# Kernel tuning notes

Measured on AMD Instinct MI355X. Metric: run time of the kernel, lower is better.

The kernel has to match this reference:

```python
import jax, jax.numpy as jnp
import numpy as np

NB = 5  # frequency bands


def _ln(x, g, b, eps=1e-5):
    m = jnp.mean(x, axis=-1, keepdims=True)
    v = jnp.var(x, axis=-1, keepdims=True)
    return (x - m) / jnp.sqrt(v + eps) * g + b


def _graph_adj(x, adj_w, sw1, sb1, sw2, sb2, pos_factor, pos_enc):
    # x: [B, D, N] -> degree-normalized adjacency [B, N, N]
    d = x.shape[1]
    xt = jnp.swapaxes(x, 1, 2)  # [B, N, D]
    # concat-MLP first layer split: cat(xi, xj) @ W1 == xi @ W1[:d] + xj @ W1[d:]
    a = xt @ sw1[:d]
    bpart = xt @ sw1[d:]
    h = jax.nn.elu(a[:, :, None, :] + bpart[:, None, :, :] + sb1)  # [B, N, N, H]
    dyn = jax.nn.sigmoid(jnp.squeeze(h @ sw2, -1) + sb2)  # [B, N, N]
    static = jax.nn.softmax(adj_w, axis=-1)
    pos = jax.nn.softmax(pos_enc, axis=-1)
    comb = jax.nn.softmax(static + dyn + pos_factor * pos, axis=-1)
    deg = jnp.sum(comb, axis=-1)
    dis = (deg + 1e-8) ** -0.5
    return dis[:, :, None] * comb * dis[:, None, :]


def _gcn(x, adj, w, b):
    # x: [B, D, N], adj: [B, N, N] -> [B, D_out, N]
    xt = jnp.swapaxes(x, 1, 2)
    out = jnp.einsum('bij,bjd->bid', adj, xt) @ w + b
    return jnp.swapaxes(out, 1, 2)


def _mha(x, qkv_w, qkv_b, ow, ob, nh=4):
    B, S, D = x.shape
    dh = D // nh
    q, k, v = jnp.split(x @ qkv_w + qkv_b, 3, axis=-1)
    q = q.reshape(B, S, nh, dh)
    k = k.reshape(B, S, nh, dh)
    v = v.reshape(B, S, nh, dh)
    att = jax.nn.softmax(jnp.einsum('bihd,bjhd->bhij', q, k) / float(np.sqrt(dh)), axis=-1)
    o = jnp.einsum('bhij,bjhd->bihd', att, v).reshape(B, S, D)
    return o @ ow + ob


def setup_inputs():
    key = jax.random.key(0)
    B, D, N = 16, 256, 64
    ks = iter(jax.random.split(key, 40))

    def rn(shape, s=0.05):
        return jax.random.normal(next(ks), shape, dtype=jnp.float32) * s

    eyeN = jnp.eye(N, dtype=jnp.float32)
    return dict(
        feature=jax.random.normal(next(ks), (B, NB * D, 1, N), dtype=jnp.float32),
        l_adj_w=jnp.tile(eyeN[None], (NB, 1, 1)),
        l_sim_w1=rn((NB, 2 * D, D)), l_sim_b1=jnp.zeros((NB, D), jnp.float32),
        l_sim_w2=rn((NB, D, 1)), l_sim_b2=jnp.zeros((NB, 1), jnp.float32),
        l_pos_factor=jnp.full((NB,), 0.5, jnp.float32),
        l_pos_enc=jnp.tile(eyeN[None], (NB, 1, 1)),
        l_gcn_w=rn((NB, D, D)), l_gcn_b=jnp.zeros((NB, D), jnp.float32),
        g_adj_w=jnp.eye(NB, dtype=jnp.float32),
        g_sim_w1=rn((2 * D, D)), g_sim_b1=jnp.zeros((D,), jnp.float32),
        g_sim_w2=rn((D, 1)), g_sim_b2=jnp.zeros((1,), jnp.float32),
        g_pos_factor=jnp.float32(0.5),
        g_pos_enc=jnp.eye(NB, dtype=jnp.float32),
        g_gcn_w=rn((D, D)), g_gcn_b=jnp.zeros((D,), jnp.float32),
        qkv_w=rn((D, 3 * D)), qkv_b=jnp.zeros((3 * D,), jnp.float32),
        attn_ow=rn((D, D)), attn_ob=jnp.zeros((D,), jnp.float32),
        ln1_g=jnp.ones((D,), jnp.float32), ln1_b=jnp.zeros((D,), jnp.float32),
        ln2_g=jnp.ones((D,), jnp.float32), ln2_b=jnp.zeros((D,), jnp.float32),
        mlp_w1=rn((D, 4 * D)), mlp_b1=jnp.zeros((4 * D,), jnp.float32),
        mlp_w2=rn((4 * D, D)), mlp_b2=jnp.zeros((D,), jnp.float32),
        imp_w=rn((NB, N, 1)), imp_b=jnp.zeros((NB, 1), jnp.float32),
    )


def reference(feature, l_adj_w, l_sim_w1, l_sim_b1, l_sim_w2, l_sim_b2,
              l_pos_factor, l_pos_enc, l_gcn_w, l_gcn_b,
              g_adj_w, g_sim_w1, g_sim_b1, g_sim_w2, g_sim_b2,
              g_pos_factor, g_pos_enc, g_gcn_w, g_gcn_b,
              qkv_w, qkv_b, attn_ow, attn_ob,
              ln1_g, ln1_b, ln2_g, ln2_b,
              mlp_w1, mlp_b1, mlp_w2, mlp_b2,
              imp_w, imp_b):
    B = feature.shape[0]
    D = l_gcn_w.shape[-1]
    N = feature.shape[-1]
    # [B, 5*D, 1, N] -> [5, B, D, N] band-major
    x5 = jnp.moveaxis(feature.reshape(B, NB, D, N), 1, 0)
    # per-band local graphs + GCNs (vmapped over the 5 bands)
    local_adj = jax.vmap(_graph_adj)(x5, l_adj_w, l_sim_w1, l_sim_b1,
                                     l_sim_w2, l_sim_b2, l_pos_factor, l_pos_enc)
    local_out = jax.vmap(_gcn)(x5, local_adj, l_gcn_w, l_gcn_b)  # [5, B, D, N]
    scale_nodes = jnp.moveaxis(jnp.mean(local_out, axis=-1), 0, 1)  # [B, 5, D]
    # cross-band attention block (pre: MHA + residual + LN, then MLP + residual + LN)
    attn = _mha(scale_nodes, qkv_w, qkv_b, attn_ow, attn_ob)
    h1 = _ln(scale_nodes + attn, ln1_g, ln1_b)
    mlp = jax.nn.gelu(h1 @ mlp_w1 + mlp_b1, approximate=False) @ mlp_w2 + mlp_b2
    se = _ln(h1 + mlp, ln2_g, ln2_b)  # [B, 5, D]
    # global scale graph over the 5 band nodes
    xg = jnp.swapaxes(se, 1, 2)  # [B, D, 5]
    g_adj = _graph_adj(xg, g_adj_w, g_sim_w1, g_sim_b1, g_sim_w2, g_sim_b2,
                       g_pos_factor, g_pos_enc)
    g_out = jnp.swapaxes(_gcn(xg, g_adj, g_gcn_w, g_gcn_b), 1, 2)  # [B, 5, D]
    # modulate each local band feature by its global scale vector
    enh = local_out * jnp.moveaxis(g_out, 1, 0)[..., None]  # [5, B, D, N]
    # per-band importance projection over channels: [5, B, D, 1]
    out5 = jnp.einsum('kbdn,kno->kbdo', enh, imp_w) + imp_b[:, None, None, :]
    output = jnp.moveaxis(out5, 0, 1).reshape(B, NB * D, 1, 1)
    return output, g_adj, jnp.moveaxis(local_out, 0, 1)
```

## Files before the change

kernel.cpp:

```cpp
#include <hip/hip_runtime.h>
#include <hip/hip_bf16.h>

#define NBANDS 5
#define BATCH  16
#define DIM    256
#define NNODE  64
#define SEQ    5

typedef __hip_bfloat16 bf16;
typedef unsigned short ushort_t;
typedef __attribute__((ext_vector_type(8))) short short8;
typedef __attribute__((ext_vector_type(4))) float float4v;

#define MFMA __builtin_amdgcn_mfma_f32_16x16x32_bf16

__device__ __forceinline__ float bu2f(ushort_t u){
    bf16 h = *reinterpret_cast<bf16*>(&u);
    return __bfloat162float(h);
}
__device__ __forceinline__ ushort_t f2bu(float x){
    bf16 h = __float2bfloat16(x);
    return *reinterpret_cast<ushort_t*>(&h);
}
__device__ __forceinline__ float elu(float v){
    return (v > 0.f) ? v : (__expf(v) - 1.f);
}

__global__ void __launch_bounds__(256) k_head(
    const float* __restrict__ l_adj_w, const float* __restrict__ l_pos_enc,
    const float* __restrict__ l_pf,
    const float* __restrict__ g_adj_w, const float* __restrict__ g_pos_enc,
    const float* __restrict__ g_pf,
    float* __restrict__ sbase, float* __restrict__ gbase,
    const float* __restrict__ w1, const float* __restrict__ gw,
    ushort_t* __restrict__ w1bt, ushort_t* __restrict__ gwbt)
{
    int blk = blockIdx.x;
    int tid = threadIdx.x;
    __shared__ ushort_t tile[64][65];

    if (blk < 80) {
        int r = blk*4 + (tid>>6);
        int k = r >> 6, i = r & 63;
        int t = tid & 63;
        float aw = l_adj_w[(k*NNODE + i)*NNODE + t];
        float pe = l_pos_enc[(k*NNODE + i)*NNODE + t];
        float m1 = aw, m2 = pe;
        for (int o=32;o>0;o>>=1){ m1 = fmaxf(m1, __shfl_xor(m1,o,64)); m2 = fmaxf(m2, __shfl_xor(m2,o,64)); }
        float e1 = __expf(aw-m1), e2 = __expf(pe-m2);
        float s1=e1, s2=e2;
        for (int o=32;o>0;o>>=1){ s1 += __shfl_xor(s1,o,64); s2 += __shfl_xor(s2,o,64); }
        float pf = l_pf[k];
        sbase[(k*NNODE+i)*NNODE + t] = e1/s1 + pf*(e2/s2);
    } else if (blk == 80) {
        if (tid < NBANDS) {
            int i = tid;
            float r1[NBANDS], r2[NBANDS];
            float m1=-1e30f, m2=-1e30f;
            for (int j=0;j<NBANDS;j++){
                r1[j]=g_adj_w[i*NBANDS+j]; r2[j]=g_pos_enc[i*NBANDS+j];
                m1=fmaxf(m1,r1[j]); m2=fmaxf(m2,r2[j]);
            }
            float s1=0.f,s2=0.f;
            for (int j=0;j<NBANDS;j++){ r1[j]=__expf(r1[j]-m1); r2[j]=__expf(r2[j]-m2); s1+=r1[j]; s2+=r2[j]; }
            float pf = g_pf[0];
            for (int j=0;j<NBANDS;j++) gbase[i*NBANDS+j] = r1[j]/s1 + pf*(r2[j]/s2);
        }
    } else {
        int idx = blk - 81;
        int inst = idx >> 4;
        int t = idx & 15;
        int r0 = (t>>2)*64, c0 = (t&3)*64;
        const float* src; ushort_t* dst;
        if (inst < 10){
            int k = inst>>1, half = inst&1;
            src = w1  + ((size_t)k*512 + half*256)*256;
            dst = w1bt+ ((size_t)k*512 + half*256)*256;
        } else {
            int k = inst-10;
            src = gw  + (size_t)k*65536;
            dst = gwbt+ (size_t)k*65536;
        }
        int jj = tid & 63, i4 = tid >> 6;
        for (int p=0;p<16;p++){
            int i = p*4 + i4;
            tile[i][jj] = f2bu(src[(size_t)(r0+i)*256 + c0 + jj]);
        }
        __syncthreads();
        for (int p=0;p<16;p++){
            int i = p*4 + i4;
            dst[(size_t)(c0+i)*256 + r0 + jj] = tile[jj][i];
        }
    }
}

__global__ void __launch_bounds__(512) k_graph(
    const float* __restrict__ feat,
    const ushort_t* __restrict__ w1bt, const float* __restrict__ b1,
    const float* __restrict__ w2, const float* __restrict__ b2arr,
    const float* __restrict__ sbase,
    const ushort_t* __restrict__ gwbt, const float* __restrict__ gb,
    const float* __restrict__ imp_w,
    float* __restrict__ out_local,
    float* __restrict__ scalew4, float* __restrict__ impw4)
{
    int kb = blockIdx.x % 80;
    int iq = blockIdx.x / 80;
    int k  = kb >> 4;
    int b  = kb & 15;
    int i0 = iq << 4;
    int tid = threadIdx.x;
    int w = tid >> 6, lane = tid & 63, c16 = lane & 15, quad = lane >> 4;

    __shared__ ushort_t Ubuf[64*266 + 8];
    __shared__ ushort_t as[16][264];
    __shared__ ushort_t cs[16][72];
    __shared__ ushort_t ys[16][264];
    __shared__ float w2s[DIM];

    const float* src = feat + ((size_t)b*NBANDS + k)*DIM*NNODE;

    int il0 = w*2, il1 = w*2 + 1;
    float sb0 = sbase[(k*NNODE + i0 + il0)*NNODE + lane];
    float sb1 = sbase[(k*NNODE + i0 + il1)*NNODE + lane];
    float sbias2 = b2arr[k];

    if (tid < DIM) w2s[tid] = w2[k*DIM + tid];
    #pragma unroll
    for (int u = 0; u < 32; ++u){
        int idx = u*512 + tid;
        Ubuf[(idx & 63)*264 + (idx >> 6)] = f2bu(src[idx]);
    }
    __syncthreads();

    int col0 = w*32 + c16;
    int col1 = col0 + 16;

    const ushort_t* Ba = w1bt + (size_t)k*512*DIM;
    const ushort_t* Bb = Ba + 256*DIM;
    float4v z = {0.f,0.f,0.f,0.f};
    float4v aA0=z, aA1=z;
    float4v aB00=z,aB01=z,aB10=z,aB11=z,aB20=z,aB21=z,aB30=z,aB31=z;
    #pragma unroll
    for (int ks = 0; ks < 8; ++ks){
        int ko = ks*32 + quad*8;
        short8 fa = *reinterpret_cast<const short8*>(&Ubuf[(i0 + c16)*264 + ko]);
        short8 f0 = *reinterpret_cast<const short8*>(&Ubuf[( 0 + c16)*264 + ko]);
        short8 f1 = *reinterpret_cast<const short8*>(&Ubuf[(16 + c16)*264 + ko]);
        short8 f2 = *reinterpret_cast<const short8*>(&Ubuf[(32 + c16)*264 + ko]);
        short8 f3 = *reinterpret_cast<const short8*>(&Ubuf[(48 + c16)*264 + ko]);
        short8 wa0 = *reinterpret_cast<const short8*>(Ba + (size_t)col0*DIM + ko);
        short8 wa1 = *reinterpret_cast<const short8*>(Ba + (size_t)col1*DIM + ko);
        short8 wb0 = *reinterpret_cast<const short8*>(Bb + (size_t)col0*DIM + ko);
        short8 wb1 = *reinterpret_cast<const short8*>(Bb + (size_t)col1*DIM + ko);
        aA0  = MFMA(fa, wa0, aA0, 0,0,0);
        aA1  = MFMA(fa, wa1, aA1, 0,0,0);
        aB00 = MFMA(f0, wb0, aB00, 0,0,0);
        aB01 = MFMA(f0, wb1, aB01, 0,0,0);
        aB10 = MFMA(f1, wb0, aB10, 0,0,0);
        aB11 = MFMA(f1, wb1, aB11, 0,0,0);
        aB20 = MFMA(f2, wb0, aB20, 0,0,0);
        aB21 = MFMA(f2, wb1, aB21, 0,0,0);
        aB30 = MFMA(f3, wb0, aB30, 0,0,0);
        aB31 = MFMA(f3, wb1, aB31, 0,0,0);
    }
    __syncthreads();
    {
        float bias0 = b1[k*DIM + col0];
        float bias1 = b1[k*DIM + col1];
        int r0 = quad*4;
        #pragma unroll
        for (int r = 0; r < 4; ++r){
            as[r0 + r][col0] = f2bu(aA0[r] + bias0);
            as[r0 + r][col1] = f2bu(aA1[r] + bias1);
            Ubuf[( 0 + r0 + r)*266 + col0] = f2bu(aB00[r]);
            Ubuf[( 0 + r0 + r)*266 + col1] = f2bu(aB01[r]);
            Ubuf[(16 + r0 + r)*266 + col0] = f2bu(aB10[r]);
            Ubuf[(16 + r0 + r)*266 + col1] = f2bu(aB11[r]);
            Ubuf[(32 + r0 + r)*266 + col0] = f2bu(aB20[r]);
            Ubuf[(32 + r0 + r)*266 + col1] = f2bu(aB21[r]);
            Ubuf[(48 + r0 + r)*266 + col0] = f2bu(aB30[r]);
            Ubuf[(48 + r0 + r)*266 + col1] = f2bu(aB31[r]);
        }
    }
    __syncthreads();

    {
        const ushort_t* bd = Ubuf + 266*lane;
        const ushort_t* a0p = as[il0];
        const ushort_t* a1p = as[il1];
        float acc0 = 0.f, acc1 = 0.f;
        #pragma unroll 4
        for (int dd = 0; dd < 64; ++dd){
            unsigned int blo = *reinterpret_cast<const unsigned int*>(bd + dd*4);
            unsigned int bhi = *reinterpret_cast<const unsigned int*>(bd + dd*4 + 2);
            ushort4 a0 = *reinterpret_cast<const ushort4*>(a0p + dd*4);
            ushort4 a1 = *reinterpret_cast<const ushort4*>(a1p + dd*4);
            float4 wv  = *reinterpret_cast<const float4*>(&w2s[dd*4]);
            float bx = bu2f((ushort_t)(blo & 0xffffu));
            float by = bu2f((ushort_t)(blo >> 16));
            float bz = bu2f((ushort_t)(bhi & 0xffffu));
            float bq = bu2f((ushort_t)(bhi >> 16));
            acc0 += elu(bu2f(a0.x)+bx)*wv.x + elu(bu2f(a0.y)+by)*wv.y
                  + elu(bu2f(a0.z)+bz)*wv.z + elu(bu2f(a0.w)+bq)*wv.w;
            acc1 += elu(bu2f(a1.x)+bx)*wv.x + elu(bu2f(a1.y)+by)*wv.y
                  + elu(bu2f(a1.z)+bz)*wv.z + elu(bu2f(a1.w)+bq)*wv.w;
        }
        float sg0 = 1.f/(1.f + __expf(-(acc0 + sbias2)));
        float sg1 = 1.f/(1.f + __expf(-(acc1 + sbias2)));
        float val0 = sb0 + sg0;
        float val1 = sb1 + sg1;
        float m0 = val0, m1 = val1;
        for (int o=32;o>0;o>>=1){ m0 = fmaxf(m0, __shfl_xor(m0,o,64)); m1 = fmaxf(m1, __shfl_xor(m1,o,64)); }
        float e0 = __expf(val0 - m0), e1 = __expf(val1 - m1);
        float s0 = e0, s1 = e1;
        for (int o=32;o>0;o>>=1){ s0 += __shfl_xor(s0,o,64); s1 += __shfl_xor(s1,o,64); }
        cs[il0][lane] = f2bu(e0/s0);
        cs[il1][lane] = f2bu(e1/s1);
    }
    __syncthreads();

    float4v aY0 = z, aY1 = z;
    {
        #pragma unroll
        for (int ks = 0; ks < 2; ++ks){
            int ko = ks*32 + quad*8;
            short8 af = *reinterpret_cast<const short8*>(&cs[c16][ko]);
            const float* f0p = src + (size_t)col0*NNODE + ko;
            const float* f1p = src + (size_t)col1*NNODE + ko;
            float4 x0 = *reinterpret_cast<const float4*>(f0p);
            float4 x1 = *reinterpret_cast<const float4*>(f0p+4);
            float4 y0 = *reinterpret_cast<const float4*>(f1p);
            float4 y1 = *reinterpret_cast<const float4*>(f1p+4);
            short8 bf0, bf1;
            bf0[0]=(short)f2bu(x0.x); bf0[1]=(short)f2bu(x0.y); bf0[2]=(short)f2bu(x0.z); bf0[3]=(short)f2bu(x0.w);
            bf0[4]=(short)f2bu(x1.x); bf0[5]=(short)f2bu(x1.y); bf0[6]=(short)f2bu(x1.z); bf0[7]=(short)f2bu(x1.w);
            bf1[0]=(short)f2bu(y0.x); bf1[1]=(short)f2bu(y0.y); bf1[2]=(short)f2bu(y0.z); bf1[3]=(short)f2bu(y0.w);
            bf1[4]=(short)f2bu(y1.x); bf1[5]=(short)f2bu(y1.y); bf1[6]=(short)f2bu(y1.z); bf1[7]=(short)f2bu(y1.w);
            aY0 = MFMA(af, bf0, aY0, 0,0,0);
            aY1 = MFMA(af, bf1, aY1, 0,0,0);
        }
        #pragma unroll
        for (int r=0;r<4;++r){
            ys[quad*4 + r][col0] = f2bu(aY0[r]);
            ys[quad*4 + r][col1] = f2bu(aY1[r]);
        }
    }
    __syncthreads();

    {
        float4v aG0 = z, aG1 = z;
        const ushort_t* Bg = gwbt + (size_t)k*DIM*DIM;
        #pragma unroll
        for (int ks = 0; ks < 8; ++ks){
            int ko = ks*32 + quad*8;
            short8 af = *reinterpret_cast<const short8*>(&ys[c16][ko]);
            short8 g0 = *reinterpret_cast<const short8*>(Bg + (size_t)col0*DIM + ko);
            short8 g1 = *reinterpret_cast<const short8*>(Bg + (size_t)col1*DIM + ko);
            aG0 = MFMA(af, g0, aG0, 0,0,0);
            aG1 = MFMA(af, g1, aG1, 0,0,0);
        }
        int nb = i0 + quad*4;
        float iw0 = imp_w[k*NNODE + nb + 0];
        float iw1 = imp_w[k*NNODE + nb + 1];
        float iw2 = imp_w[k*NNODE + nb + 2];
        float iw3 = imp_w[k*NNODE + nb + 3];
        size_t obase = ((size_t)b*NBANDS + k)*DIM;

        float bias0 = gb[k*DIM + col0];
        float v0 = aG0[0]+bias0, v1 = aG0[1]+bias0, v2 = aG0[2]+bias0, v3 = aG0[3]+bias0;
        float4 vv = make_float4(v0,v1,v2,v3);
        *reinterpret_cast<float4*>(&out_local[(obase + col0)*NNODE + nb]) = vv;
        float s  = v0+v1+v2+v3;
        float di = v0*iw0 + v1*iw1 + v2*iw2 + v3*iw3;
        s  += __shfl_xor(s,16,64);  s  += __shfl_xor(s,32,64);
        di += __shfl_xor(di,16,64); di += __shfl_xor(di,32,64);
        if (quad == 0){
            size_t o = ((size_t)iq*80 + b*SEQ + k)*DIM + col0;
            scalew4[o] = s;
            impw4[o]   = di;
        }

        float bias1 = gb[k*DIM + col1];
        v0 = aG1[0]+bias1; v1 = aG1[1]+bias1; v2 = aG1[2]+bias1; v3 = aG1[3]+bias1;
        vv = make_float4(v0,v1,v2,v3);
        *reinterpret_cast<float4*>(&out_local[(obase + col1)*NNODE + nb]) = vv;
        s  = v0+v1+v2+v3;
        di = v0*iw0 + v1*iw1 + v2*iw2 + v3*iw3;
        s  += __shfl_xor(s,16,64);  s  += __shfl_xor(s,32,64);
        di += __shfl_xor(di,16,64); di += __shfl_xor(di,32,64);
        if (quad == 0){
            size_t o = ((size_t)iq*80 + b*SEQ + k)*DIM + col1;
            scalew4[o] = s;
            impw4[o]   = di;
        }
    }
}

__global__ void __launch_bounds__(256) k_qkv_gemv(const float* __restrict__ scalew4,
                        const float* __restrict__ w, const float* __restrict__ bias,
                        float* __restrict__ out)
{
    int row = blockIdx.x / 12;
    int n0 = (blockIdx.x % 12) * 64;
    int tid = threadIdx.x;
    int c = tid & 63, s = tid >> 6;
    __shared__ float xs[DIM];
    __shared__ float part[4][64];
    {
        size_t basei = (size_t)row*DIM + tid;
        xs[tid] = (scalew4[basei] + scalew4[20480 + basei]
                 + scalew4[40960 + basei] + scalew4[61440 + basei]) * (1.f/64.f);
    }
    __syncthreads();
    const float* wp = w + (size_t)(s*64)*768 + n0 + c;
    const float* xp = xs + s*64;
    float acc = 0.f;
    #pragma unroll 8
    for (int i = 0; i < 64; ++i) acc += xp[i] * wp[(size_t)i*768];
    part[s][c] = acc;
    __syncthreads();
    if (s == 0){
        out[(size_t)row*768 + n0 + c] = bias[n0+c] + part[0][c]+part[1][c]+part[2][c]+part[3][c];
    }
}

template<int COLS, int SLICES>
__global__ void __launch_bounds__(256) k_gemv(const float* __restrict__ x, const float* __restrict__ w,
                       const float* __restrict__ bias, float* __restrict__ out,
                       int K, int N, int act)
{
    int chunks = N / COLS;
    int row = blockIdx.x / chunks;
    int n0 = (blockIdx.x % chunks) * COLS;
    int c = threadIdx.x % COLS, s = threadIdx.x / COLS;
    __shared__ float xs[1024];
    __shared__ float part[SLICES][COLS];
    for (int i = threadIdx.x; i < K; i += 256) xs[i] = x[(size_t)row*K + i];
    __syncthreads();
    int klen = K / SLICES;
    const float* wp = w + (size_t)(s*klen)*N + n0 + c;
    const float* xp = xs + s*klen;
    float acc = 0.f;
    #pragma unroll 8
    for (int i = 0; i < klen; ++i) acc += xp[i] * wp[(size_t)i*N];
    part[s][c] = acc;
    __syncthreads();
    if (s == 0){
        float v = bias[n0+c];
        #pragma unroll
        for (int q=0;q<SLICES;q++) v += part[q][c];
        if (act) v = 0.5f*v*(1.f + erff(v*0.70710678118654752f));
        out[(size_t)row*N + n0 + c] = v;
    }
}

__global__ void __launch_bounds__(256) k_projattn(const float* __restrict__ qkvw,
                        const float* __restrict__ ow, const float* __restrict__ ob,
                        float* __restrict__ projw)
{
    int row = blockIdx.x / 4;
    int n0 = (blockIdx.x % 4) * 64;
    int b = row / SEQ, i = row % SEQ;
    int tid = threadIdx.x;
    int h = tid >> 6, l = tid & 63;
    __shared__ float xs[DIM];
    __shared__ float part[4][64];
    const float* base = qkvw + (size_t)b*SEQ*3*DIM;
    float qv = base[(size_t)i*3*DIM + h*64 + l];
    float pj[SEQ];
    #pragma unroll
    for (int j=0;j<SEQ;j++){
        float p = qv * base[(size_t)j*3*DIM + DIM + h*64 + l];
        for (int o=32;o>0;o>>=1) p += __shfl_xor(p,o,64);
        pj[j] = p * 0.125f;
    }
    float m = pj[0];
    #pragma unroll
    for (int j=1;j<SEQ;j++) m = fmaxf(m, pj[j]);
    float ssum = 0.f;
    #pragma unroll
    for (int j=0;j<SEQ;j++){ pj[j] = __expf(pj[j]-m); ssum += pj[j]; }
    float inv = 1.f/ssum;
    float o = 0.f;
    #pragma unroll
    for (int j=0;j<SEQ;j++) o += pj[j]*inv * base[(size_t)j*3*DIM + 2*DIM + h*64 + l];
    xs[tid] = o;
    __syncthreads();
    int c = tid & 63, s = tid >> 6;
    const float* wp = ow + (size_t)(s*64)*DIM + n0 + c;
    const float* xp = xs + s*64;
    float acc = 0.f;
    #pragma unroll 8
    for (int k=0;k<64;++k) acc += xp[k] * wp[(size_t)k*DIM];
    part[s][c] = acc;
    __syncthreads();
    if (s == 0){
        projw[(size_t)row*DIM + n0 + c] = ob[n0+c] + part[0][c]+part[1][c]+part[2][c]+part[3][c];
    }
}

__device__ __forceinline__ float block_ln(float v, int tid, float* red, float g, float bln)
{
    float s = v;
    for (int o=32;o>0;o>>=1) s += __shfl_xor(s,o,64);
    int wave = tid>>6, lane = tid&63;
    if (lane==0) red[wave] = s;
    __syncthreads();
    float mean = (red[0]+red[1]+red[2]+red[3]) * (1.f/DIM);
    float c = v - mean;
    float q = c*c;
    for (int o=32;o>0;o>>=1) q += __shfl_xor(q,o,64);
    __syncthreads();
    if (lane==0) red[wave] = q;
    __syncthreads();
    float var = (red[0]+red[1]+red[2]+red[3]) * (1.f/DIM);
    return c * rsqrtf(var + 1e-5f) * g + bln;
}

__global__ void __launch_bounds__(256) k_mlp1_ln(const float* __restrict__ projw,
                         const float* __restrict__ scalew4,
                         const float* __restrict__ ln1_g, const float* __restrict__ ln1_b,
                         const float* __restrict__ w1, const float* __restrict__ b1,
                         float* __restrict__ h1w, float* __restrict__ mhw)
{
    int row = blockIdx.x / 16;
    int n0 = (blockIdx.x % 16) * 64;
    int tid = threadIdx.x;
    __shared__ float xs[DIM];
    __shared__ float red[4];
    __shared__ float part[4][64];
    size_t basei = (size_t)row*DIM + tid;
    float sc = (scalew4[basei] + scalew4[20480 + basei]
              + scalew4[40960 + basei] + scalew4[61440 + basei]) * (1.f/64.f);
    float v = projw[basei] + sc;
    float h = block_ln(v, tid, red, ln1_g[tid], ln1_b[tid]);
    xs[tid] = h;
    if ((blockIdx.x % 16) == 0) h1w[basei] = h;
    __syncthreads();
    int c = tid & 63, s = tid >> 6;
    const float* wp = w1 + (size_t)(s*64)*1024 + n0 + c;
    const float* xp = xs + s*64;
    float acc = 0.f;
    #pragma unroll 8
    for (int i=0;i<64;++i) acc += xp[i] * wp[(size_t)i*1024];
    part[s][c] = acc;
    __syncthreads();
    if (s == 0){
        float o = b1[n0+c] + part[0][c] + part[1][c] + part[2][c] + part[3][c];
        o = 0.5f*o*(1.f + erff(o*0.70710678118654752f));
        mhw[(size_t)row*1024 + n0 + c] = o;
    }
}

__global__ void __launch_bounds__(256) k_gab_ln(const float* __restrict__ m2w,
                        const float* __restrict__ h1w,
                        const float* __restrict__ ln2_g, const float* __restrict__ ln2_b,
                        const float* __restrict__ gw1, const float* __restrict__ gb1,
                        float* __restrict__ sew, float* __restrict__ gaw, float* __restrict__ gbw)
{
    int row = blockIdx.x / 4;
    int n0 = (blockIdx.x % 4) * 64;
    int tid = threadIdx.x;
    __shared__ float xs[DIM];
    __shared__ float red[4];
    __shared__ float partA[4][64];
    __shared__ float partB[4][64];
    float v = m2w[(size_t)row*DIM + tid] + h1w[(size_t)row*DIM + tid];
    float h = block_ln(v, tid, red, ln2_g[tid], ln2_b[tid]);
    xs[tid] = h;
    if ((blockIdx.x % 4) == 0) sew[(size_t)row*DIM + tid] = h;
    __syncthreads();
    int c = tid & 63, s = tid >> 6;
    const float* wpA = gw1 + (size_t)(s*64)*DIM + n0 + c;
    const float* wpB = wpA + (size_t)DIM*DIM;
    const float* xp = xs + s*64;
    float aA = 0.f, aB = 0.f;
    #pragma unroll 8
    for (int i=0;i<64;++i){
        float xv = xp[i];
        aA += xv * wpA[(size_t)i*DIM];
        aB += xv * wpB[(size_t)i*DIM];
    }
    partA[s][c] = aA;
    partB[s][c] = aB;
    __syncthreads();
    if (s == 0){
        gaw[(size_t)row*DIM + n0 + c] = gb1[n0+c] + partA[0][c]+partA[1][c]+partA[2][c]+partA[3][c];
        gbw[(size_t)row*DIM + n0 + c] = partB[0][c]+partB[1][c]+partB[2][c]+partB[3][c];
    }
}

__global__ void __launch_bounds__(256) k_goutfin(const float* __restrict__ gaw,
                        const float* __restrict__ gbw,
                        const float* __restrict__ gw2, const float* __restrict__ gb2,
                        const float* __restrict__ gbase,
                        const float* __restrict__ sew,
                        const float* __restrict__ ggw, const float* __restrict__ ggb,
                        const float* __restrict__ impw4, const float* __restrict__ imp_b,
                        float* __restrict__ out0, float* __restrict__ out_gadj)
{
    int row = blockIdx.x / 4;
    int n0 = (blockIdx.x % 4) * 64;
    int b = row / SEQ, i = row % SEQ;
    int tid = threadIdx.x;
    int wave = tid >> 6, lane = tid & 63;
    __shared__ float dyn_s[SEQ];
    __shared__ float xs[DIM];
    __shared__ float part[4][64];
    for (int j = wave; j < SEQ; j += 4){
        const float* gar = gaw + (size_t)row*DIM;
        const float* gbr = gbw + ((size_t)b*SEQ + j)*DIM;
        float acc = 0.f;
        #pragma unroll
        for (int m=0;m<4;m++){
            int dd = lane + m*64;
            float v = gar[dd] + gbr[dd];
            acc += elu(v) * gw2[dd];
        }
        for (int o=32;o>0;o>>=1) acc += __shfl_xor(acc,o,64);
        if (lane==0) dyn_s[j] = acc;
    }
    __syncthreads();
    float gc[SEQ];
    {
        float sb2 = gb2[0];
        float m = -1e30f;
        #pragma unroll
        for (int j=0;j<SEQ;j++){
            float sg = 1.f/(1.f+__expf(-(dyn_s[j]+sb2)));
            gc[j] = gbase[i*SEQ+j] + sg;
            m = fmaxf(m, gc[j]);
        }
        float ssum=0.f;
        #pragma unroll
        for (int j=0;j<SEQ;j++){ gc[j]=__expf(gc[j]-m); ssum+=gc[j]; }
        float inv = 1.f/ssum;
        #pragma unroll
        for (int j=0;j<SEQ;j++) gc[j] *= inv;
    }
    if (n0 == 0 && tid < SEQ) out_gadj[((size_t)b*SEQ+i)*SEQ + tid] = gc[tid];
    float t = 0.f;
    #pragma unroll
    for (int j=0;j<SEQ;j++) t += gc[j]*sew[((size_t)b*SEQ + j)*DIM + tid];
    xs[tid] = t;
    __syncthreads();
    int c = tid & 63, s = tid >> 6;
    const float* wp = ggw + (size_t)(s*64)*DIM + n0 + c;
    const float* xp = xs + s*64;
    float acc = 0.f;
    #pragma unroll 8
    for (int k=0;k<64;++k) acc += xp[k] * wp[(size_t)k*DIM];
    part[s][c] = acc;
    __syncthreads();
    if (s == 0){
        float g = ggb[n0+c] + part[0][c]+part[1][c]+part[2][c]+part[3][c];
        size_t o = (size_t)row*DIM + n0 + c;
        float imps = impw4[o] + impw4[20480 + o] + impw4[40960 + o] + impw4[61440 + o];
        out0[o] = g * imps + imp_b[i];
    }
}

extern "C" void kernel_launch(void* const* d_in, const int* in_sizes, int n_in,
                              void* d_out, int out_size, void* d_ws, size_t ws_size,
                              hipStream_t stream)
{
    const float* feature      = (const float*)d_in[0];
    const float* l_adj_w      = (const float*)d_in[1];
    const float* l_sim_w1     = (const float*)d_in[2];
    const float* l_sim_b1     = (const float*)d_in[3];
    const float* l_sim_w2     = (const float*)d_in[4];
    const float* l_sim_b2     = (const float*)d_in[5];
    const float* l_pos_factor = (const float*)d_in[6];
    const float* l_pos_enc    = (const float*)d_in[7];
    const float* l_gcn_w      = (const float*)d_in[8];
    const float* l_gcn_b      = (const float*)d_in[9];
    const float* g_adj_w      = (const float*)d_in[10];
    const float* g_sim_w1     = (const float*)d_in[11];
    const float* g_sim_b1     = (const float*)d_in[12];
    const float* g_sim_w2     = (const float*)d_in[13];
    const float* g_sim_b2     = (const float*)d_in[14];
    const float* g_pos_factor = (const float*)d_in[15];
    const float* g_pos_enc    = (const float*)d_in[16];
    const float* g_gcn_w      = (const float*)d_in[17];
    const float* g_gcn_b      = (const float*)d_in[18];
    const float* qkv_w        = (const float*)d_in[19];
    const float* qkv_b        = (const float*)d_in[20];
    const float* attn_ow      = (const float*)d_in[21];
    const float* attn_ob      = (const float*)d_in[22];
    const float* ln1_g        = (const float*)d_in[23];
    const float* ln1_b        = (const float*)d_in[24];
    const float* ln2_g        = (const float*)d_in[25];
    const float* ln2_b        = (const float*)d_in[26];
    const float* mlp_w1       = (const float*)d_in[27];
    const float* mlp_b1       = (const float*)d_in[28];
    const float* mlp_w2       = (const float*)d_in[29];
    const float* mlp_b2       = (const float*)d_in[30];
    const float* imp_w        = (const float*)d_in[31];
    const float* imp_b        = (const float*)d_in[32];

    float* out0      = (float*)d_out;
    float* out_gadj  = out0 + (size_t)BATCH*NBANDS*DIM;
    float* out_local = out_gadj + (size_t)BATCH*NBANDS*NBANDS;

    ushort_t* w1bt = (ushort_t*)d_ws;
    ushort_t* gwbt = w1bt + (size_t)NBANDS*512*DIM;
    float* fp = (float*)(gwbt + (size_t)NBANDS*DIM*DIM);
    float* sbase   = fp; fp += NBANDS*NNODE*NNODE;
    float* gbase   = fp; fp += 32;
    float* scalew4 = fp; fp += 4*BATCH*SEQ*DIM;
    float* impw4   = fp; fp += 4*BATCH*SEQ*DIM;
    float* qkvw    = fp; fp += BATCH*SEQ*3*DIM;
    float* projw   = fp; fp += BATCH*SEQ*DIM;
    float* h1w     = fp; fp += BATCH*SEQ*DIM;
    float* mhw     = fp; fp += BATCH*SEQ*4*DIM;
    float* m2w     = fp; fp += BATCH*SEQ*DIM;
    float* sew     = fp; fp += BATCH*SEQ*DIM;
    float* gaw     = fp; fp += BATCH*SEQ*DIM;
    float* gbw     = fp; fp += BATCH*SEQ*DIM;

    const int ROWS = BATCH*SEQ;

    k_head<<<321, 256, 0, stream>>>(l_adj_w, l_pos_enc, l_pos_factor,
                                    g_adj_w, g_pos_enc, g_pos_factor,
                                    sbase, gbase,
                                    l_sim_w1, l_gcn_w, w1bt, gwbt);
    k_graph<<<NBANDS*BATCH*4, 512, 0, stream>>>(feature, w1bt, l_sim_b1,
                                    l_sim_w2, l_sim_b2, sbase,
                                    gwbt, l_gcn_b, imp_w,
                                    out_local, scalew4, impw4);
    k_qkv_gemv<<<ROWS*12, 256, 0, stream>>>(scalew4, qkv_w, qkv_b, qkvw);
    k_projattn<<<ROWS*4, 256, 0, stream>>>(qkvw, attn_ow, attn_ob, projw);
    k_mlp1_ln<<<ROWS*16, 256, 0, stream>>>(projw, scalew4, ln1_g, ln1_b, mlp_w1, mlp_b1, h1w, mhw);
    k_gemv<32,8><<<ROWS*8, 256, 0, stream>>>(mhw, mlp_w2, mlp_b2, m2w, 1024, 256, 0);
    k_gab_ln<<<ROWS*4, 256, 0, stream>>>(m2w, h1w, ln2_g, ln2_b, g_sim_w1, g_sim_b1, sew, gaw, gbw);
    k_goutfin<<<ROWS*4, 256, 0, stream>>>(gaw, gbw, g_sim_w2, g_sim_b2, gbase,
                                          sew, g_gcn_w, g_gcn_b, impw4, imp_b,
                                          out0, out_gadj);
}
```

Measured before the change: 215.8 us.

## Fuse attention, MLP and layer-norm chain into one per-row kernel

Five small GEMV kernels (QKV, attention+proj, MLP1+LN, MLP2, LN2+graph projection) are merged into one kernel with one 512-thread block per sequence row, and their intermediates stay in shared memory. In k_graph, ys now reuses Ubuf, w2 is read straight from global memory, and the feature transpose load packs 8 bf16 values per store. This removes four launches and their global round trips. The cost is only 80 blocks doing full-width GEMVs with K-loops up to 256 long, so parallelism drops sharply and weight reads are repeated per row.

```diff
diff --git a/kernel.cpp b/kernel.cpp
--- a/kernel.cpp
+++ b/kernel.cpp
@@ -24,6 +24,9 @@
 }
 __device__ __forceinline__ float elu(float v){
     return (v > 0.f) ? v : (__expf(v) - 1.f);
+}
+__device__ __forceinline__ float sum4(const float* __restrict__ p, size_t i){
+    return p[i] + p[20480 + i] + p[40960 + i] + p[61440 + i];
 }
 
 __global__ void __launch_bounds__(256) k_head(
@@ -112,11 +115,10 @@
     int tid = threadIdx.x;
     int w = tid >> 6, lane = tid & 63, c16 = lane & 15, quad = lane >> 4;
 
-    __shared__ ushort_t Ubuf[64*266 + 8];
-    __shared__ ushort_t as[16][264];
-    __shared__ ushort_t cs[16][72];
-    __shared__ ushort_t ys[16][264];
-    __shared__ float w2s[DIM];
+    __shared__ __align__(16) ushort_t Ubuf[64*266 + 8];
+    __shared__ __align__(16) ushort_t as[16][260];
+    __shared__ __align__(16) ushort_t cs[16][72];
+    ushort_t* ys = Ubuf;
 
     const float* src = feat + ((size_t)b*NBANDS + k)*DIM*NNODE;
 
@@ -125,11 +127,15 @@
     float sb1 = sbase[(k*NNODE + i0 + il1)*NNODE + lane];
     float sbias2 = b2arr[k];
 
-    if (tid < DIM) w2s[tid] = w2[k*DIM + tid];
     #pragma unroll
-    for (int u = 0; u < 32; ++u){
-        int idx = u*512 + tid;
-        Ubuf[(idx & 63)*264 + (idx >> 6)] = f2bu(src[idx]);
+    for (int u = 0; u < 4; ++u){
+        int t = u*512 + tid;
+        int n = t & 63;
+        int d0 = (t >> 6) * 8;
+        short8 pk;
+        #pragma unroll
+        for (int i = 0; i < 8; ++i) pk[i] = (short)f2bu(src[(size_t)(d0+i)*NNODE + n]);
+        *reinterpret_cast<short8*>(&Ubuf[(size_t)n*264 + d0]) = pk;
     }
     __syncthreads();
 
@@ -187,8 +193,9 @@
 
     {
         const ushort_t* bd = Ubuf + 266*lane;
-        const ushort_t* a0p = as[il0];
-        const ushort_t* a1p = as[il1];
+        const ushort_t* a0p = &as[il0][0];
+        const ushort_t* a1p = &as[il1][0];
+        const float* w2p = w2 + k*DIM;
         float acc0 = 0.f, acc1 = 0.f;
         #pragma unroll 4
         for (int dd = 0; dd < 64; ++dd){
@@ -196,7 +203,7 @@
             unsigned int bhi = *reinterpret_cast<const unsigned int*>(bd + dd*4 + 2);
             ushort4 a0 = *reinterpret_cast<const ushort4*>(a0p + dd*4);
             ushort4 a1 = *reinterpret_cast<const ushort4*>(a1p + dd*4);
-            float4 wv  = *reinterpret_cast<const float4*>(&w2s[dd*4]);
+            float4 wv  = *reinterpret_cast<const float4*>(w2p + dd*4);
             float bx = bu2f((ushort_t)(blo & 0xffffu));
             float by = bu2f((ushort_t)(blo >> 16));
             float bz = bu2f((ushort_t)(bhi & 0xffffu));
@@ -220,8 +227,8 @@
     }
     __syncthreads();
 
-    float4v aY0 = z, aY1 = z;
-    {
+    {
+        float4v aY0 = z, aY1 = z;
         #pragma unroll
         for (int ks = 0; ks < 2; ++ks){
             int ko = ks*32 + quad*8;
@@ -242,8 +249,8 @@
         }
         #pragma unroll
         for (int r=0;r<4;++r){
-            ys[quad*4 + r][col0] = f2bu(aY0[r]);
-            ys[quad*4 + r][col1] = f2bu(aY1[r]);
+            ys[(quad*4 + r)*264 + col0] = f2bu(aY0[r]);
+            ys[(quad*4 + r)*264 + col1] = f2bu(aY1[r]);
         }
     }
     __syncthreads();
@@ -254,7 +261,7 @@
         #pragma unroll
         for (int ks = 0; ks < 8; ++ks){
             int ko = ks*32 + quad*8;
-            short8 af = *reinterpret_cast<const short8*>(&ys[c16][ko]);
+            short8 af = *reinterpret_cast<const short8*>(&ys[c16*264 + ko]);
             short8 g0 = *reinterpret_cast<const short8*>(Bg + (size_t)col0*DIM + ko);
             short8 g1 = *reinterpret_cast<const short8*>(Bg + (size_t)col1*DIM + ko);
             aG0 = MFMA(af, g0, aG0, 0,0,0);
@@ -269,225 +276,181 @@
 
         float bias0 = gb[k*DIM + col0];
         float v0 = aG0[0]+bias0, v1 = aG0[1]+bias0, v2 = aG0[2]+bias0, v3 = aG0[3]+bias0;
-        float4 vv = make_float4(v0,v1,v2,v3);
-        *reinterpret_cast<float4*>(&out_local[(obase + col0)*NNODE + nb]) = vv;
+        *reinterpret_cast<float4*>(&out_local[(obase + col0)*NNODE + nb]) =
+            make_float4(v0,v1,v2,v3);
         float s  = v0+v1+v2+v3;
         float di = v0*iw0 + v1*iw1 + v2*iw2 + v3*iw3;
         s  += __shfl_xor(s,16,64);  s  += __shfl_xor(s,32,64);
         di += __shfl_xor(di,16,64); di += __shfl_xor(di,32,64);
         if (quad == 0){
-            size_t o = ((size_t)iq*80 + b*SEQ + k)*DIM + col0;
+            size_t o = (size_t)iq*20480 + ((size_t)b*SEQ + k)*DIM + col0;
             scalew4[o] = s;
             impw4[o]   = di;
         }
 
         float bias1 = gb[k*DIM + col1];
         v0 = aG1[0]+bias1; v1 = aG1[1]+bias1; v2 = aG1[2]+bias1; v3 = aG1[3]+bias1;
-        vv = make_float4(v0,v1,v2,v3);
-        *reinterpret_cast<float4*>(&out_local[(obase + col1)*NNODE + nb]) = vv;
+        *reinterpret_cast<float4*>(&out_local[(obase + col1)*NNODE + nb]) =
+            make_float4(v0,v1,v2,v3);
         s  = v0+v1+v2+v3;
         di = v0*iw0 + v1*iw1 + v2*iw2 + v3*iw3;
         s  += __shfl_xor(s,16,64);  s  += __shfl_xor(s,32,64);
         di += __shfl_xor(di,16,64); di += __shfl_xor(di,32,64);
         if (quad == 0){
-            size_t o = ((size_t)iq*80 + b*SEQ + k)*DIM + col1;
+            size_t o = (size_t)iq*20480 + ((size_t)b*SEQ + k)*DIM + col1;
             scalew4[o] = s;
             impw4[o]   = di;
         }
     }
 }
 
-__global__ void __launch_bounds__(256) k_qkv_gemv(const float* __restrict__ scalew4,
-                        const float* __restrict__ w, const float* __restrict__ bias,
-                        float* __restrict__ out)
-{
-    int row = blockIdx.x / 12;
-    int n0 = (blockIdx.x % 12) * 64;
-    int tid = threadIdx.x;
-    int c = tid & 63, s = tid >> 6;
-    __shared__ float xs[DIM];
-    __shared__ float part[4][64];
-    {
-        size_t basei = (size_t)row*DIM + tid;
-        xs[tid] = (scalew4[basei] + scalew4[20480 + basei]
-                 + scalew4[40960 + basei] + scalew4[61440 + basei]) * (1.f/64.f);
-    }
-    __syncthreads();
-    const float* wp = w + (size_t)(s*64)*768 + n0 + c;
-    const float* xp = xs + s*64;
-    float acc = 0.f;
-    #pragma unroll 8
-    for (int i = 0; i < 64; ++i) acc += xp[i] * wp[(size_t)i*768];
-    part[s][c] = acc;
-    __syncthreads();
-    if (s == 0){
-        out[(size_t)row*768 + n0 + c] = bias[n0+c] + part[0][c]+part[1][c]+part[2][c]+part[3][c];
-    }
-}
-
-template<int COLS, int SLICES>
-__global__ void __launch_bounds__(256) k_gemv(const float* __restrict__ x, const float* __restrict__ w,
-                       const float* __restrict__ bias, float* __restrict__ out,
-                       int K, int N, int act)
-{
-    int chunks = N / COLS;
-    int row = blockIdx.x / chunks;
-    int n0 = (blockIdx.x % chunks) * COLS;
-    int c = threadIdx.x % COLS, s = threadIdx.x / COLS;
-    __shared__ float xs[1024];
-    __shared__ float part[SLICES][COLS];
-    for (int i = threadIdx.x; i < K; i += 256) xs[i] = x[(size_t)row*K + i];
-    __syncthreads();
-    int klen = K / SLICES;
-    const float* wp = w + (size_t)(s*klen)*N + n0 + c;
-    const float* xp = xs + s*klen;
-    float acc = 0.f;
-    #pragma unroll 8
-    for (int i = 0; i < klen; ++i) acc += xp[i] * wp[(size_t)i*N];
-    part[s][c] = acc;
-    __syncthreads();
-    if (s == 0){
-        float v = bias[n0+c];
-        #pragma unroll
-        for (int q=0;q<SLICES;q++) v += part[q][c];
-        if (act) v = 0.5f*v*(1.f + erff(v*0.70710678118654752f));
-        out[(size_t)row*N + n0 + c] = v;
-    }
-}
-
-__global__ void __launch_bounds__(256) k_projattn(const float* __restrict__ qkvw,
-                        const float* __restrict__ ow, const float* __restrict__ ob,
-                        float* __restrict__ projw)
-{
-    int row = blockIdx.x / 4;
-    int n0 = (blockIdx.x % 4) * 64;
-    int b = row / SEQ, i = row % SEQ;
-    int tid = threadIdx.x;
-    int h = tid >> 6, l = tid & 63;
-    __shared__ float xs[DIM];
-    __shared__ float part[4][64];
-    const float* base = qkvw + (size_t)b*SEQ*3*DIM;
-    float qv = base[(size_t)i*3*DIM + h*64 + l];
-    float pj[SEQ];
-    #pragma unroll
-    for (int j=0;j<SEQ;j++){
-        float p = qv * base[(size_t)j*3*DIM + DIM + h*64 + l];
-        for (int o=32;o>0;o>>=1) p += __shfl_xor(p,o,64);
-        pj[j] = p * 0.125f;
-    }
-    float m = pj[0];
-    #pragma unroll
-    for (int j=1;j<SEQ;j++) m = fmaxf(m, pj[j]);
-    float ssum = 0.f;
-    #pragma unroll
-    for (int j=0;j<SEQ;j++){ pj[j] = __expf(pj[j]-m); ssum += pj[j]; }
-    float inv = 1.f/ssum;
-    float o = 0.f;
-    #pragma unroll
-    for (int j=0;j<SEQ;j++) o += pj[j]*inv * base[(size_t)j*3*DIM + 2*DIM + h*64 + l];
-    xs[tid] = o;
-    __syncthreads();
-    int c = tid & 63, s = tid >> 6;
-    const float* wp = ow + (size_t)(s*64)*DIM + n0 + c;
-    const float* xp = xs + s*64;
-    float acc = 0.f;
-    #pragma unroll 8
-    for (int k=0;k<64;++k) acc += xp[k] * wp[(size_t)k*DIM];
-    part[s][c] = acc;
-    __syncthreads();
-    if (s == 0){
-        projw[(size_t)row*DIM + n0 + c] = ob[n0+c] + part[0][c]+part[1][c]+part[2][c]+part[3][c];
-    }
-}
-
-__device__ __forceinline__ float block_ln(float v, int tid, float* red, float g, float bln)
+__device__ __forceinline__ float block_ln512(float v, int tid, float* red, float g, float bb)
 {
     float s = v;
     for (int o=32;o>0;o>>=1) s += __shfl_xor(s,o,64);
     int wave = tid>>6, lane = tid&63;
     if (lane==0) red[wave] = s;
     __syncthreads();
-    float mean = (red[0]+red[1]+red[2]+red[3]) * (1.f/DIM);
+    float mean = (red[0]+red[1]+red[2]+red[3]+red[4]+red[5]+red[6]+red[7]) * (1.f/512.f);
     float c = v - mean;
     float q = c*c;
     for (int o=32;o>0;o>>=1) q += __shfl_xor(q,o,64);
     __syncthreads();
     if (lane==0) red[wave] = q;
     __syncthreads();
-    float var = (red[0]+red[1]+red[2]+red[3]) * (1.f/DIM);
-    return c * rsqrtf(var + 1e-5f) * g + bln;
-}
-
-__global__ void __launch_bounds__(256) k_mlp1_ln(const float* __restrict__ projw,
-                         const float* __restrict__ scalew4,
-                         const float* __restrict__ ln1_g, const float* __restrict__ ln1_b,
-                         const float* __restrict__ w1, const float* __restrict__ b1,
-                         float* __restrict__ h1w, float* __restrict__ mhw)
+    float var = (red[0]+red[1]+red[2]+red[3]+red[4]+red[5]+red[6]+red[7]) * (1.f/512.f);
+    return c * rsqrtf(var + 1e-5f) * g + bb;
+}
+
+__global__ void __launch_bounds__(512) k_attnmlp(
+    const float* __restrict__ scalew4,
+    const float* __restrict__ qkv_w, const float* __restrict__ qkv_b,
+    const float* __restrict__ attn_ow, const float* __restrict__ attn_ob,
+    const float* __restrict__ ln1_g, const float* __restrict__ ln1_b,
+    const float* __restrict__ mlp_w1, const float* __restrict__ mlp_b1,
+    const float* __restrict__ mlp_w2, const float* __restrict__ mlp_b2,
+    const float* __restrict__ ln2_g, const float* __restrict__ ln2_b,
+    const float* __restrict__ gw1, const float* __restrict__ gb1,
+    float* __restrict__ sew, float* __restrict__ gaw, float* __restrict__ gbw)
 {
-    int row = blockIdx.x / 16;
-    int n0 = (blockIdx.x % 16) * 64;
+    int r = blockIdx.x;
+    int b = r / SEQ, i = r % SEQ;
     int tid = threadIdx.x;
-    __shared__ float xs[DIM];
-    __shared__ float red[4];
-    __shared__ float part[4][64];
-    size_t basei = (size_t)row*DIM + tid;
-    float sc = (scalew4[basei] + scalew4[20480 + basei]
-              + scalew4[40960 + basei] + scalew4[61440 + basei]) * (1.f/64.f);
-    float v = projw[basei] + sc;
-    float h = block_ln(v, tid, red, ln1_g[tid], ln1_b[tid]);
-    xs[tid] = h;
-    if ((blockIdx.x % 16) == 0) h1w[basei] = h;
-    __syncthreads();
-    int c = tid & 63, s = tid >> 6;
-    const float* wp = w1 + (size_t)(s*64)*1024 + n0 + c;
-    const float* xp = xs + s*64;
-    float acc = 0.f;
-    #pragma unroll 8
-    for (int i=0;i<64;++i) acc += xp[i] * wp[(size_t)i*1024];
-    part[s][c] = acc;
-    __syncthreads();
-    if (s == 0){
-        float o = b1[n0+c] + part[0][c] + part[1][c] + part[2][c] + part[3][c];
-        o = 0.5f*o*(1.f + erff(o*0.70710678118654752f));
-        mhw[(size_t)row*1024 + n0 + c] = o;
-    }
-}
-
-__global__ void __launch_bounds__(256) k_gab_ln(const float* __restrict__ m2w,
-                        const float* __restrict__ h1w,
-                        const float* __restrict__ ln2_g, const float* __restrict__ ln2_b,
-                        const float* __restrict__ gw1, const float* __restrict__ gb1,
-                        float* __restrict__ sew, float* __restrict__ gaw, float* __restrict__ gbw)
-{
-    int row = blockIdx.x / 4;
-    int n0 = (blockIdx.x % 4) * 64;
-    int tid = threadIdx.x;
-    __shared__ float xs[DIM];
-    __shared__ float red[4];
-    __shared__ float partA[4][64];
-    __shared__ float partB[4][64];
-    float v = m2w[(size_t)row*DIM + tid] + h1w[(size_t)row*DIM + tid];
-    float h = block_ln(v, tid, red, ln2_g[tid], ln2_b[tid]);
-    xs[tid] = h;
-    if ((blockIdx.x % 4) == 0) sew[(size_t)row*DIM + tid] = h;
-    __syncthreads();
-    int c = tid & 63, s = tid >> 6;
-    const float* wpA = gw1 + (size_t)(s*64)*DIM + n0 + c;
-    const float* wpB = wpA + (size_t)DIM*DIM;
-    const float* xp = xs + s*64;
-    float aA = 0.f, aB = 0.f;
-    #pragma unroll 8
-    for (int i=0;i<64;++i){
-        float xv = xp[i];
-        aA += xv * wpA[(size_t)i*DIM];
-        aB += xv * wpB[(size_t)i*DIM];
-    }
-    partA[s][c] = aA;
-    partB[s][c] = aB;
-    __syncthreads();
-    if (s == 0){
-        gaw[(size_t)row*DIM + n0 + c] = gb1[n0+c] + partA[0][c]+partA[1][c]+partA[2][c]+partA[3][c];
-        gbw[(size_t)row*DIM + n0 + c] = partB[0][c]+partB[1][c]+partB[2][c]+partB[3][c];
+    int wave = tid >> 6, lane = tid & 63;
+
+    __shared__ float xs5[SEQ][260];
+    __shared__ float kv[2*SEQ][260];
+    __shared__ float qi[260];
+    __shared__ float xo[260];
+    __shared__ float h1s[260];
+    __shared__ float mh[1032];
+    __shared__ float ses[260];
+    __shared__ float parts[2][260];
+    __shared__ float red[8];
+
+    for (int t = tid; t < SEQ*DIM; t += 512){
+        int j = t >> 8, d = t & 255;
+        xs5[j][d] = sum4(scalew4, ((size_t)b*SEQ + j)*DIM + d) * (1.f/64.f);
+    }
+    __syncthreads();
+
+    for (int o = tid; o < 2816; o += 512){
+        int row, colIdx; float* dst;
+        if (o < 256){ row = i; colIdx = o; dst = &qi[o]; }
+        else {
+            int o2 = o - 256;
+            int j = o2 >> 9, c = o2 & 511;
+            row = j; colIdx = 256 + c;
+            dst = (c < 256) ? &kv[j][c] : &kv[SEQ + j][c - 256];
+        }
+        float acc = qkv_b[colIdx];
+        const float* wp = qkv_w + colIdx;
+        const float* xp = xs5[row];
+        #pragma unroll 8
+        for (int d = 0; d < DIM; ++d) acc += xp[d] * wp[(size_t)d*768];
+        *dst = acc;
+    }
+    __syncthreads();
+
+    if (wave < 4){
+        int h = wave;
+        float qv = qi[h*64 + lane];
+        float pj[SEQ];
+        #pragma unroll
+        for (int j=0;j<SEQ;j++){
+            float p = qv * kv[j][h*64 + lane];
+            for (int o=32;o>0;o>>=1) p += __shfl_xor(p,o,64);
+            pj[j] = p * 0.125f;
+        }
+        float m = pj[0];
+        #pragma unroll
+        for (int j=1;j<SEQ;j++) m = fmaxf(m, pj[j]);
+        float ss = 0.f;
+        #pragma unroll
+        for (int j=0;j<SEQ;j++){ pj[j] = __expf(pj[j]-m); ss += pj[j]; }
+        float inv = 1.f/ss;
+        float o = 0.f;
+        #pragma unroll
+        for (int j=0;j<SEQ;j++) o += pj[j]*inv * kv[SEQ + j][h*64 + lane];
+        xo[h*64 + lane] = o;
+    }
+    __syncthreads();
+
+    {
+        int c = tid & 255, s = tid >> 8;
+        const float* wp = attn_ow + (size_t)(s*128)*DIM + c;
+        const float* xp = xo + s*128;
+        float acc = 0.f;
+        #pragma unroll 8
+        for (int kk=0;kk<128;++kk) acc += xp[kk] * wp[(size_t)kk*DIM];
+        parts[s][c] = acc;
+    }
+    __syncthreads();
+    if (tid < 256) h1s[tid] = attn_ob[tid] + parts[0][tid] + parts[1][tid] + xs5[i][tid];
+    __syncthreads();
+    {
+        int c = tid & 255;
+        float h = block_ln512(h1s[c], tid, red, ln1_g[c], ln1_b[c]);
+        if (tid < 256) h1s[c] = h;
+    }
+    __syncthreads();
+
+    for (int o = tid; o < 1024; o += 512){
+        float acc = mlp_b1[o];
+        const float* wp = mlp_w1 + o;
+        #pragma unroll 8
+        for (int d = 0; d < DIM; ++d) acc += h1s[d] * wp[(size_t)d*1024];
+        mh[o] = 0.5f*acc*(1.f + erff(acc*0.70710678118654752f));
+    }
+    __syncthreads();
+
+    {
+        int c = tid & 255, s = tid >> 8;
+        const float* wp = mlp_w2 + (size_t)(s*512)*DIM + c;
+        const float* xp = mh + s*512;
+        float acc = 0.f;
+        #pragma unroll 8
+        for (int kk=0;kk<512;++kk) acc += xp[kk] * wp[(size_t)kk*DIM];
+        parts[s][c] = acc;
+    }
+    __syncthreads();
+    if (tid < 256) ses[tid] = mlp_b2[tid] + parts[0][tid] + parts[1][tid] + h1s[tid];
+    __syncthreads();
+    {
+        int c = tid & 255;
+        float h = block_ln512(ses[c], tid, red, ln2_g[c], ln2_b[c]);
+        if (tid < 256){ ses[c] = h; sew[(size_t)r*DIM + c] = h; }
+    }
+    __syncthreads();
+
+    {
+        int mat = tid >> 8, c = tid & 255;
+        float acc = (mat == 0) ? gb1[c] : 0.f;
+        const float* wp = gw1 + (size_t)(mat*DIM)*DIM + c;
+        #pragma unroll 8
+        for (int d = 0; d < DIM; ++d) acc += ses[d] * wp[(size_t)d*DIM];
+        if (mat == 0) gaw[(size_t)r*DIM + c] = acc;
+        else          gbw[(size_t)r*DIM + c] = acc;
     }
 }
 
@@ -556,7 +519,7 @@
     if (s == 0){
         float g = ggb[n0+c] + part[0][c]+part[1][c]+part[2][c]+part[3][c];
         size_t o = (size_t)row*DIM + n0 + c;
-        float imps = impw4[o] + impw4[20480 + o] + impw4[40960 + o] + impw4[61440 + o];
+        float imps = sum4(impw4, o);
         out0[o] = g * imps + imp_b[i];
     }
 }
@@ -610,11 +573,6 @@
     float* gbase   = fp; fp += 32;
     float* scalew4 = fp; fp += 4*BATCH*SEQ*DIM;
     float* impw4   = fp; fp += 4*BATCH*SEQ*DIM;
-    float* qkvw    = fp; fp += BATCH*SEQ*3*DIM;
-    float* projw   = fp; fp += BATCH*SEQ*DIM;
-    float* h1w     = fp; fp += BATCH*SEQ*DIM;
-    float* mhw     = fp; fp += BATCH*SEQ*4*DIM;
-    float* m2w     = fp; fp += BATCH*SEQ*DIM;
     float* sew     = fp; fp += BATCH*SEQ*DIM;
     float* gaw     = fp; fp += BATCH*SEQ*DIM;
     float* gbw     = fp; fp += BATCH*SEQ*DIM;
@@ -629,11 +587,11 @@
                                     l_sim_w2, l_sim_b2, sbase,
                                     gwbt, l_gcn_b, imp_w,
                                     out_local, scalew4, impw4);
-    k_qkv_gemv<<<ROWS*12, 256, 0, stream>>>(scalew4, qkv_w, qkv_b, qkvw);
-    k_projattn<<<ROWS*4, 256, 0, stream>>>(qkvw, attn_ow, attn_ob, projw);
-    k_mlp1_ln<<<ROWS*16, 256, 0, stream>>>(projw, scalew4, ln1_g, ln1_b, mlp_w1, mlp_b1, h1w, mhw);
-    k_gemv<32,8><<<ROWS*8, 256, 0, stream>>>(mhw, mlp_w2, mlp_b2, m2w, 1024, 256, 0);
-    k_gab_ln<<<ROWS*4, 256, 0, stream>>>(m2w, h1w, ln2_g, ln2_b, g_sim_w1, g_sim_b1, sew, gaw, gbw);
+    k_attnmlp<<<ROWS, 512, 0, stream>>>(scalew4, qkv_w, qkv_b,
+                                    attn_ow, attn_ob, ln1_g, ln1_b,
+                                    mlp_w1, mlp_b1, mlp_w2, mlp_b2,
+                                    ln2_g, ln2_b, g_sim_w1, g_sim_b1,
+                                    sew, gaw, gbw);
     k_goutfin<<<ROWS*4, 256, 0, stream>>>(gaw, gbw, g_sim_w2, g_sim_b2, gbase,
                                           sew, g_gcn_w, g_gcn_b, impw4, imp_b,
                                           out0, out_gadj);
```

New measurement: 291.4 us. 1.35x slower.
